# Kernel tuning notes

Measured on AMD Instinct MI355X. Metric: run time of the kernel, lower is better.

## Reference

```python
import jax, jax.numpy as jnp
import numpy as np

N_NODES = 50000
N_EDGES = 800000
N_GRAPHS = 256
D_IN, D_H1, D_H2, D_OUT = 64, 64, 64, 64


def gcn_conv(x, W, b, src, dst, n_nodes):
    # PyG GCNConv (eval): h = x @ W; add self-loops; deg[i] = in_deg(i) + 1;
    # out[i] = sum_{j->i} h[j] * deg[i]^-1/2 deg[j]^-1/2 + h[i]/deg[i] + b
    h = x @ W  # [N, F]
    ones = jnp.ones((src.shape[0],), dtype=x.dtype)
    deg = jax.ops.segment_sum(ones, dst, num_segments=n_nodes) + 1.0  # self loop
    dinv = jax.lax.rsqrt(deg)
    norm = dinv[src] * dinv[dst]  # [E]
    msg = h[src] * norm[:, None]  # [E, F]  (memory-bound gather)
    agg = jax.ops.segment_sum(msg, dst, num_segments=n_nodes)  # scatter-add
    agg = agg + h * (1.0 / deg)[:, None]  # self-loop contribution
    return agg + b


def setup_inputs() -> dict:
    key = jax.random.key(0)
    ks = jax.random.split(key, 12)
    x = jax.random.normal(ks[0], (N_NODES, D_IN), dtype=jnp.float32)
    src = jax.random.randint(ks[1], (N_EDGES,), 0, N_NODES)
    dst = jax.random.randint(ks[2], (N_EDGES,), 0, N_NODES)
    batch = jnp.sort(jax.random.randint(ks[3], (N_NODES,), 0, N_GRAPHS))
    def glorot(k, fin, fout):
        s = jnp.sqrt(6.0 / (fin + fout))
        return jax.random.uniform(k, (fin, fout), jnp.float32, -s, s)
    return {
        "x": x, "src": src, "dst": dst, "batch": batch,
        "W1": glorot(ks[4], D_IN, D_H1), "b1": jnp.zeros((D_H1,), jnp.float32),
        "W2": glorot(ks[5], D_H1, D_H2), "b2": jnp.zeros((D_H2,), jnp.float32),
        "W3": glorot(ks[6], D_H2, D_OUT), "b3": jnp.zeros((D_OUT,), jnp.float32),
        "Wl": glorot(ks[7], D_OUT, 1), "bl": jnp.zeros((1,), jnp.float32),
    }


def reference(x, src, dst, batch, W1, b1, W2, b2, W3, b3, Wl, bl):
    n = x.shape[0]
    h = jax.nn.relu(gcn_conv(x, W1, b1, src, dst, n))   # dropout inactive (eval)
    h = jax.nn.relu(gcn_conv(h, W2, b2, src, dst, n))
    h = jax.nn.relu(gcn_conv(h, W3, b3, src, dst, n))
    # global_mean_pool over graph ids
    sums = jax.ops.segment_sum(h, batch, num_segments=N_GRAPHS)  # [G, F]
    cnt = jax.ops.segment_sum(jnp.ones((n,), h.dtype), batch, num_segments=N_GRAPHS)
    pooled = sums / jnp.maximum(cnt, 1.0)[:, None]
    return pooled @ Wl + bl  # [G, 1]
```

## Files before the change

### kernel.cpp

```cpp
#include <hip/hip_runtime.h>

#define N_NODES 50000
#define N_EDGES 800000
#define N_GRAPHS 256
#define F 64
#define NBUCK 196
#define CAP 5120
#define P3_TILE 2048
#define P3_GRID ((N_EDGES + P3_TILE - 1) / P3_TILE)
#define BCAP 6144
#define ZOFF (N_NODES * 128)

__device__ __forceinline__ unsigned short f2bf(float f) {
    union { float f; unsigned u; } c; c.f = f;
    unsigned u = c.u + 0x7FFFu + ((c.u >> 16) & 1u);
    return (unsigned short)(u >> 16);
}
__device__ __forceinline__ unsigned pack2bf(float lo, float hi) {
    return (unsigned)f2bf(lo) | ((unsigned)f2bf(hi) << 16);
}
__device__ __forceinline__ float bfl(unsigned u) {
    union { unsigned u; float f; } c; c.u = u << 16; return c.f;
}
__device__ __forceinline__ float bfh(unsigned u) {
    union { unsigned u; float f; } c; c.u = u & 0xFFFF0000u; return c.f;
}

__global__ __launch_bounds__(256) void partition_edges(const int* __restrict__ src,
                                                       const int* __restrict__ dst,
                                                       int* __restrict__ bcur,
                                                       unsigned int* __restrict__ bpair) {
    __shared__ int bh[NBUCK], bloc[NBUCK], bpos[NBUCK];
    int t = threadIdx.x;
    int lo = blockIdx.x * P3_TILE;
    int hi = min(lo + P3_TILE, N_EDGES);
    for (int i = t; i < NBUCK; i += 256) { bh[i] = 0; bpos[i] = 0; }
    __syncthreads();
    for (int e = lo + t; e < hi; e += 256) atomicAdd(&bh[dst[e] >> 8], 1);
    __syncthreads();
    for (int i = t; i < NBUCK; i += 256)
        bloc[i] = bh[i] ? atomicAdd(&bcur[i], bh[i]) : 0;
    __syncthreads();
    for (int e = lo + t; e < hi; e += 256) {
        int d = dst[e];
        int b = d >> 8;
        int r = atomicAdd(&bpos[b], 1);
        bpair[(size_t)b * CAP + bloc[b] + r] = ((unsigned)src[e] << 8) | (unsigned)(d & 255);
    }
}

__global__ __launch_bounds__(256) void bucket_sort(const unsigned int* __restrict__ bpair,
                                                   const int* __restrict__ bcur,
                                                   int* __restrict__ eidx,
                                                   int* __restrict__ rbeg,
                                                   int* __restrict__ rend,
                                                   float* __restrict__ dinv,
                                                   unsigned short* __restrict__ Abf) {
    __shared__ int cnt[256], s[256], pos[256];
    __shared__ int lout[BCAP];
    int b = blockIdx.x, t = threadIdx.x;
    int base = b * CAP;
    int sz = bcur[b];

    if (b == 0 && t < 8) ((uint4*)Abf)[(size_t)N_NODES * 8 + t] = make_uint4(0u, 0u, 0u, 0u);

    cnt[t] = 0;
    __syncthreads();
    for (int i = t; i < sz; i += 256) atomicAdd(&cnt[bpair[base + i] & 255], 1);
    __syncthreads();
    int v = cnt[t];
    int pv = (v + 3) & ~3;
    s[t] = pv;
    __syncthreads();
    for (int off = 1; off < 256; off <<= 1) {
        int u = (t >= off) ? s[t - off] : 0;
        __syncthreads();
        s[t] += u;
        __syncthreads();
    }
    int excl = s[t] - pv;
    pos[t] = excl;
    int node = b * 256 + t;
    if (node < N_NODES) {
        rbeg[node] = base + excl;
        rend[node] = base + excl + pv;
        dinv[node] = 1.0f / sqrtf((float)v + 1.0f);
    }
    int padtot = s[255];
    __syncthreads();

    for (int i = t; i < sz; i += 256) {
        unsigned p = bpair[base + i];
        int r = atomicAdd(&pos[p & 255], 1);
        lout[r] = (int)((p >> 8) << 7);
    }
    __syncthreads();
    for (int j = v; j < pv; j++) lout[excl + j] = ZOFF;
    __syncthreads();
    for (int i = t; i < padtot; i += 256) eidx[base + i] = lout[i];
}

#define XSTRIDE 17
template <bool BF16IN>
__global__ __launch_bounds__(256) void gemm64_t(const void* __restrict__ Xv,
                                                const float* __restrict__ W,
                                                const float* __restrict__ dinv,
                                                unsigned short* __restrict__ Hn, int n) {
    __shared__ float4 sW[64 * 16];
    __shared__ float4 sX[128 * XSTRIDE];
    int tid = threadIdx.x;
    int base = blockIdx.x * 128;

    const float4* W4 = (const float4*)W;
    for (int i = tid; i < 64 * 16; i += 256) sW[i] = W4[i];
    if (BF16IN) {
        const uint4* X4 = (const uint4*)Xv;
        for (int i = tid; i < 128 * 8; i += 256) {
            int r = i >> 3, c = i & 7;
            int node = base + r;
            uint4 u = (node < n) ? X4[(size_t)node * 8 + c]
                                 : make_uint4(0u, 0u, 0u, 0u);
            sX[r * XSTRIDE + 2 * c]     = make_float4(bfl(u.x), bfh(u.x), bfl(u.y), bfh(u.y));
            sX[r * XSTRIDE + 2 * c + 1] = make_float4(bfl(u.z), bfh(u.z), bfl(u.w), bfh(u.w));
        }
    } else {
        const float4* X4 = (const float4*)Xv;
        for (int i = tid; i < 128 * 16; i += 256) {
            int r = i >> 4, kg = i & 15;
            int node = base + r;
            sX[r * XSTRIDE + kg] = (node < n) ? X4[(size_t)node * 16 + kg]
                                              : make_float4(0.f, 0.f, 0.f, 0.f);
        }
    }
    __syncthreads();

    int fg = tid & 15;
    int ng = tid >> 4;
    float4 acc[8];
#pragma unroll
    for (int ii = 0; ii < 8; ii++) acc[ii] = make_float4(0.f, 0.f, 0.f, 0.f);

    for (int kg = 0; kg < 16; kg++) {
        float4 xv[8];
#pragma unroll
        for (int ii = 0; ii < 8; ii++) xv[ii] = sX[(ng + 16 * ii) * XSTRIDE + kg];
#pragma unroll
        for (int kk = 0; kk < 4; kk++) {
            float4 wv = sW[(4 * kg + kk) * 16 + fg];
#pragma unroll
            for (int ii = 0; ii < 8; ii++) {
                float xs = (kk == 0) ? xv[ii].x : (kk == 1) ? xv[ii].y
                         : (kk == 2) ? xv[ii].z : xv[ii].w;
                acc[ii].x += wv.x * xs;
                acc[ii].y += wv.y * xs;
                acc[ii].z += wv.z * xs;
                acc[ii].w += wv.w * xs;
            }
        }
    }

    ushort4* H4 = (ushort4*)Hn;
#pragma unroll
    for (int ii = 0; ii < 8; ii++) {
        int node = base + ng + 16 * ii;
        if (node < n) {
            float d = dinv[node];
            float4 o = acc[ii];
            ushort4 u;
            u.x = f2bf(o.x * d); u.y = f2bf(o.y * d);
            u.z = f2bf(o.z * d); u.w = f2bf(o.w * d);
            H4[(size_t)node * 16 + fg] = u;
        }
    }
}

__global__ __launch_bounds__(256) void gather_layer(const int* __restrict__ rbeg,
                                                    const int* __restrict__ rend,
                                                    const int* __restrict__ eidx,
                                                    const float* __restrict__ dinv,
                                                    const unsigned short* __restrict__ Hn,
                                                    const float* __restrict__ b,
                                                    unsigned short* __restrict__ OUT, int n) {
    int wv = (blockIdx.x * blockDim.x + threadIdx.x) >> 6;
    int lane = threadIdx.x & 63;
    int ns = lane >> 3, f = lane & 7;
    int node = wv * 8 + ns;
    bool valid = node < n;
    int beg = valid ? rbeg[node] : 0;
    int end = valid ? rend[node] : 0;
    const char* Hb = (const char*)Hn;

    float a0 = 0.f, a1 = 0.f, a2 = 0.f, a3 = 0.f;
    float a4 = 0.f, a5 = 0.f, a6 = 0.f, a7 = 0.f;
    for (int k = beg; k < end; k += 4) {
        int4 o = *(const int4*)(eidx + k);
        uint4 p = *(const uint4*)(Hb + o.x + f * 16);
        uint4 q = *(const uint4*)(Hb + o.y + f * 16);
        uint4 r = *(const uint4*)(Hb + o.z + f * 16);
        uint4 w = *(const uint4*)(Hb + o.w + f * 16);
        a0 += (bfl(p.x) + bfl(q.x)) + (bfl(r.x) + bfl(w.x));
        a1 += (bfh(p.x) + bfh(q.x)) + (bfh(r.x) + bfh(w.x));
        a2 += (bfl(p.y) + bfl(q.y)) + (bfl(r.y) + bfl(w.y));
        a3 += (bfh(p.y) + bfh(q.y)) + (bfh(r.y) + bfh(w.y));
        a4 += (bfl(p.z) + bfl(q.z)) + (bfl(r.z) + bfl(w.z));
        a5 += (bfh(p.z) + bfh(q.z)) + (bfh(r.z) + bfh(w.z));
        a6 += (bfl(p.w) + bfl(q.w)) + (bfl(r.w) + bfl(w.w));
        a7 += (bfh(p.w) + bfh(q.w)) + (bfh(r.w) + bfh(w.w));
    }

    if (valid) {
        float di = dinv[node];
        uint4 hs = *(const uint4*)(Hb + (size_t)node * 128 + f * 16);
        float4 b0 = ((const float4*)b)[2 * f];
        float4 b1 = ((const float4*)b)[2 * f + 1];
        float v0 = fmaxf(di * (a0 + bfl(hs.x)) + b0.x, 0.f);
        float v1 = fmaxf(di * (a1 + bfh(hs.x)) + b0.y, 0.f);
        float v2 = fmaxf(di * (a2 + bfl(hs.y)) + b0.z, 0.f);
        float v3 = fmaxf(di * (a3 + bfh(hs.y)) + b0.w, 0.f);
        float v4 = fmaxf(di * (a4 + bfl(hs.z)) + b1.x, 0.f);
        float v5 = fmaxf(di * (a5 + bfh(hs.z)) + b1.y, 0.f);
        float v6 = fmaxf(di * (a6 + bfl(hs.w)) + b1.z, 0.f);
        float v7 = fmaxf(di * (a7 + bfh(hs.w)) + b1.w, 0.f);
        uint4 u;
        u.x = pack2bf(v0, v1); u.y = pack2bf(v2, v3);
        u.z = pack2bf(v4, v5); u.w = pack2bf(v6, v7);
        ((uint4*)OUT)[(size_t)node * 8 + f] = u;
    }
}

__global__ __launch_bounds__(256) void gather_pool(const int* __restrict__ rbeg,
                                                   const int* __restrict__ rend,
                                                   const int* __restrict__ eidx,
                                                   const float* __restrict__ dinv,
                                                   const unsigned short* __restrict__ Hn,
                                                   const float* __restrict__ b,
                                                   const float* __restrict__ Wl,
                                                   float* __restrict__ pdot, int n) {
    int wv = (blockIdx.x * blockDim.x + threadIdx.x) >> 6;
    int lane = threadIdx.x & 63;
    int ns = lane >> 3, f = lane & 7;
    int node = wv * 8 + ns;
    bool valid = node < n;
    int beg = valid ? rbeg[node] : 0;
    int end = valid ? rend[node] : 0;
    const char* Hb = (const char*)Hn;

    float a0 = 0.f, a1 = 0.f, a2 = 0.f, a3 = 0.f;
    float a4 = 0.f, a5 = 0.f, a6 = 0.f, a7 = 0.f;
    for (int k = beg; k < end; k += 4) {
        int4 o = *(const int4*)(eidx + k);
        uint4 p = *(const uint4*)(Hb + o.x + f * 16);
        uint4 q = *(const uint4*)(Hb + o.y + f * 16);
        uint4 r = *(const uint4*)(Hb + o.z + f * 16);
        uint4 w = *(const uint4*)(Hb + o.w + f * 16);
        a0 += (bfl(p.x) + bfl(q.x)) + (bfl(r.x) + bfl(w.x));
        a1 += (bfh(p.x) + bfh(q.x)) + (bfh(r.x) + bfh(w.x));
        a2 += (bfl(p.y) + bfl(q.y)) + (bfl(r.y) + bfl(w.y));
        a3 += (bfh(p.y) + bfh(q.y)) + (bfh(r.y) + bfh(w.y));
        a4 += (bfl(p.z) + bfl(q.z)) + (bfl(r.z) + bfl(w.z));
        a5 += (bfh(p.z) + bfh(q.z)) + (bfh(r.z) + bfh(w.z));
        a6 += (bfl(p.w) + bfl(q.w)) + (bfl(r.w) + bfl(w.w));
        a7 += (bfh(p.w) + bfh(q.w)) + (bfh(r.w) + bfh(w.w));
    }

    float di = valid ? dinv[node] : 0.f;
    uint4 hs = valid ? *(const uint4*)(Hb + (size_t)node * 128 + f * 16)
                     : make_uint4(0u, 0u, 0u, 0u);
    float4 b0 = ((const float4*)b)[2 * f];
    float4 b1 = ((const float4*)b)[2 * f + 1];
    float4 w0 = ((const float4*)Wl)[2 * f];
    float4 w1 = ((const float4*)Wl)[2 * f + 1];
    float d = 0.f;
    d += fmaxf(di * (a0 + bfl(hs.x)) + b0.x, 0.f) * w0.x;
    d += fmaxf(di * (a1 + bfh(hs.x)) + b0.y, 0.f) * w0.y;
    d += fmaxf(di * (a2 + bfl(hs.y)) + b0.z, 0.f) * w0.z;
    d += fmaxf(di * (a3 + bfh(hs.y)) + b0.w, 0.f) * w0.w;
    d += fmaxf(di * (a4 + bfl(hs.z)) + b1.x, 0.f) * w1.x;
    d += fmaxf(di * (a5 + bfh(hs.z)) + b1.y, 0.f) * w1.y;
    d += fmaxf(di * (a6 + bfl(hs.w)) + b1.z, 0.f) * w1.z;
    d += fmaxf(di * (a7 + bfh(hs.w)) + b1.w, 0.f) * w1.w;
#pragma unroll
    for (int m = 1; m <= 4; m <<= 1) d += __shfl_xor(d, m);
    if (valid && f == 0) pdot[node] = d;
}

__global__ __launch_bounds__(64) void final_out(const float* __restrict__ pdot,
                                                const int* __restrict__ batch,
                                                const float* __restrict__ bl,
                                                float* __restrict__ out) {
    int g = blockIdx.x;
    __shared__ int slo, shi;
    int lane = threadIdx.x;
    if (lane == 0) {
        int a = 0, b = N_NODES;
        while (a < b) { int m = (a + b) >> 1; if (batch[m] < g) a = m + 1; else b = m; }
        slo = a;
        b = N_NODES;
        while (a < b) { int m = (a + b) >> 1; if (batch[m] < g + 1) a = m + 1; else b = m; }
        shi = a;
    }
    __syncthreads();
    int lo = slo, hi = shi;
    float acc = 0.f;
    for (int i = lo + lane; i < hi; i += 64) acc += pdot[i];
#pragma unroll
    for (int off = 32; off > 0; off >>= 1) acc += __shfl_down(acc, off);
    if (lane == 0) {
        float cnt = (float)(hi - lo);
        out[g] = acc / fmaxf(cnt, 1.0f) + bl[0];
    }
}

extern "C" void kernel_launch(void* const* d_in, const int* in_sizes, int n_in,
                              void* d_out, int out_size, void* d_ws, size_t ws_size,
                              hipStream_t stream) {
    const float* x     = (const float*)d_in[0];
    const int*   src   = (const int*)d_in[1];
    const int*   dst   = (const int*)d_in[2];
    const int*   batch = (const int*)d_in[3];
    const float* W1 = (const float*)d_in[4];  const float* b1 = (const float*)d_in[5];
    const float* W2 = (const float*)d_in[6];  const float* b2 = (const float*)d_in[7];
    const float* W3 = (const float*)d_in[8];  const float* b3 = (const float*)d_in[9];
    const float* Wl = (const float*)d_in[10]; const float* bl = (const float*)d_in[11];
    float* out = (float*)d_out;

    char* ws = (char*)d_ws;
    unsigned short* Abf = (unsigned short*)ws;
    unsigned short* Bbf = Abf + (size_t)(N_NODES + 1) * F;
    float* dinv    = (float*)(Bbf + (size_t)N_NODES * F);
    float* pdot    = dinv + N_NODES;
    int*   rbeg    = (int*)(pdot + N_NODES);
    int*   rend    = rbeg + N_NODES;
    int*   bcur    = rend + N_NODES;
    unsigned int* bpair = (unsigned int*)(bcur + NBUCK);
    int*   eidx    = (int*)(bpair + (size_t)NBUCK * CAP);

    const int GEMM_GRID   = (N_NODES + 127) / 128;
    const int GATHER_GRID = (N_NODES + 31) / 32;

    hipMemsetAsync(bcur, 0, NBUCK * sizeof(int), stream);
    partition_edges<<<P3_GRID, 256, 0, stream>>>(src, dst, bcur, bpair);
    bucket_sort<<<NBUCK, 256, 0, stream>>>(bpair, bcur, eidx, rbeg, rend, dinv, Abf);

    gemm64_t<false><<<GEMM_GRID, 256, 0, stream>>>((const void*)x, W1, dinv, Abf, N_NODES);
    gather_layer<<<GATHER_GRID, 256, 0, stream>>>(rbeg, rend, eidx, dinv, Abf, b1, Bbf, N_NODES);

    gemm64_t<true><<<GEMM_GRID, 256, 0, stream>>>((const void*)Bbf, W2, dinv, Abf, N_NODES);
    gather_layer<<<GATHER_GRID, 256, 0, stream>>>(rbeg, rend, eidx, dinv, Abf, b2, Bbf, N_NODES);

    gemm64_t<true><<<GEMM_GRID, 256, 0, stream>>>((const void*)Bbf, W3, dinv, Abf, N_NODES);
    gather_pool<<<GATHER_GRID, 256, 0, stream>>>(rbeg, rend, eidx, dinv, Abf, b3, Wl, pdot, N_NODES);

    final_out<<<N_GRAPHS, 64, 0, stream>>>(pdot, batch, bl, out);
}
```

Measured before the change: 207.1 us.

## Fuse next-layer GEMM into gather epilogue using cross-lane bpermute

Replaces the separate bf16-input GEMM kernels for layers 2 and 3 with a gather kernel that, after aggregating and applying ReLU, multiplies the node's 64 features by the next layer's weights in registers. Features are exchanged across the 8 lanes of each node with ds_bpermute, and W is staged in shared memory. This removes two kernel launches and the extra read and write of the intermediate activations. In exchange, every gather block loads W into LDS and adds 64 bpermutes plus FMAs per lane. The two feature buffers now alternate, so both need a zero padding row and the dinv offset moves accordingly.

```diff
diff --git a/kernel.cpp b/kernel.cpp
--- a/kernel.cpp
+++ b/kernel.cpp
@@ -55,14 +55,18 @@
                                                    int* __restrict__ rbeg,
                                                    int* __restrict__ rend,
                                                    float* __restrict__ dinv,
-                                                   unsigned short* __restrict__ Abf) {
+                                                   unsigned short* __restrict__ Abf,
+                                                   unsigned short* __restrict__ Bbf) {
     __shared__ int cnt[256], s[256], pos[256];
     __shared__ int lout[BCAP];
     int b = blockIdx.x, t = threadIdx.x;
     int base = b * CAP;
     int sz = bcur[b];
 
-    if (b == 0 && t < 8) ((uint4*)Abf)[(size_t)N_NODES * 8 + t] = make_uint4(0u, 0u, 0u, 0u);
+    if (b == 0 && t < 8) {
+        ((uint4*)Abf)[(size_t)N_NODES * 8 + t] = make_uint4(0u, 0u, 0u, 0u);
+        ((uint4*)Bbf)[(size_t)N_NODES * 8 + t] = make_uint4(0u, 0u, 0u, 0u);
+    }
 
     cnt[t] = 0;
     __syncthreads();
@@ -101,11 +105,10 @@
 }
 
 #define XSTRIDE 17
-template <bool BF16IN>
-__global__ __launch_bounds__(256) void gemm64_t(const void* __restrict__ Xv,
-                                                const float* __restrict__ W,
-                                                const float* __restrict__ dinv,
-                                                unsigned short* __restrict__ Hn, int n) {
+__global__ __launch_bounds__(256) void gemm64_f32(const float* __restrict__ X,
+                                                  const float* __restrict__ W,
+                                                  const float* __restrict__ dinv,
+                                                  unsigned short* __restrict__ Hn, int n) {
     __shared__ float4 sW[64 * 16];
     __shared__ float4 sX[128 * XSTRIDE];
     int tid = threadIdx.x;
@@ -113,18 +116,8 @@
 
     const float4* W4 = (const float4*)W;
     for (int i = tid; i < 64 * 16; i += 256) sW[i] = W4[i];
-    if (BF16IN) {
-        const uint4* X4 = (const uint4*)Xv;
-        for (int i = tid; i < 128 * 8; i += 256) {
-            int r = i >> 3, c = i & 7;
-            int node = base + r;
-            uint4 u = (node < n) ? X4[(size_t)node * 8 + c]
-                                 : make_uint4(0u, 0u, 0u, 0u);
-            sX[r * XSTRIDE + 2 * c]     = make_float4(bfl(u.x), bfh(u.x), bfl(u.y), bfh(u.y));
-            sX[r * XSTRIDE + 2 * c + 1] = make_float4(bfl(u.z), bfh(u.z), bfl(u.w), bfh(u.w));
-        }
-    } else {
-        const float4* X4 = (const float4*)Xv;
+    {
+        const float4* X4 = (const float4*)X;
         for (int i = tid; i < 128 * 16; i += 256) {
             int r = i >> 4, kg = i & 15;
             int node = base + r;
@@ -174,21 +167,27 @@
     }
 }
 
-__global__ __launch_bounds__(256) void gather_layer(const int* __restrict__ rbeg,
-                                                    const int* __restrict__ rend,
-                                                    const int* __restrict__ eidx,
-                                                    const float* __restrict__ dinv,
-                                                    const unsigned short* __restrict__ Hn,
-                                                    const float* __restrict__ b,
-                                                    unsigned short* __restrict__ OUT, int n) {
+__global__ __launch_bounds__(256) void gather_gemm(const int* __restrict__ rbeg,
+                                                   const int* __restrict__ rend,
+                                                   const int* __restrict__ eidx,
+                                                   const float* __restrict__ dinv,
+                                                   const unsigned short* __restrict__ Hin,
+                                                   const float* __restrict__ bias,
+                                                   const float* __restrict__ W,
+                                                   unsigned short* __restrict__ Hout, int n) {
+    __shared__ float4 sW[64 * 16];
+    const float4* W4 = (const float4*)W;
+    for (int i = threadIdx.x; i < 64 * 16; i += 256) sW[i] = W4[i];
+    __syncthreads();
+
     int wv = (blockIdx.x * blockDim.x + threadIdx.x) >> 6;
+    if (wv * 8 >= n) return;
     int lane = threadIdx.x & 63;
     int ns = lane >> 3, f = lane & 7;
     int node = wv * 8 + ns;
-    bool valid = node < n;
-    int beg = valid ? rbeg[node] : 0;
-    int end = valid ? rend[node] : 0;
-    const char* Hb = (const char*)Hn;
+    int beg = rbeg[node];
+    int end = rend[node];
+    const char* Hb = (const char*)Hin;
 
     float a0 = 0.f, a1 = 0.f, a2 = 0.f, a3 = 0.f;
     float a4 = 0.f, a5 = 0.f, a6 = 0.f, a7 = 0.f;
@@ -208,24 +207,43 @@
         a7 += (bfh(p.w) + bfh(q.w)) + (bfh(r.w) + bfh(w.w));
     }
 
-    if (valid) {
-        float di = dinv[node];
-        uint4 hs = *(const uint4*)(Hb + (size_t)node * 128 + f * 16);
-        float4 b0 = ((const float4*)b)[2 * f];
-        float4 b1 = ((const float4*)b)[2 * f + 1];
-        float v0 = fmaxf(di * (a0 + bfl(hs.x)) + b0.x, 0.f);
-        float v1 = fmaxf(di * (a1 + bfh(hs.x)) + b0.y, 0.f);
-        float v2 = fmaxf(di * (a2 + bfl(hs.y)) + b0.z, 0.f);
-        float v3 = fmaxf(di * (a3 + bfh(hs.y)) + b0.w, 0.f);
-        float v4 = fmaxf(di * (a4 + bfl(hs.z)) + b1.x, 0.f);
-        float v5 = fmaxf(di * (a5 + bfh(hs.z)) + b1.y, 0.f);
-        float v6 = fmaxf(di * (a6 + bfl(hs.w)) + b1.z, 0.f);
-        float v7 = fmaxf(di * (a7 + bfh(hs.w)) + b1.w, 0.f);
-        uint4 u;
-        u.x = pack2bf(v0, v1); u.y = pack2bf(v2, v3);
-        u.z = pack2bf(v4, v5); u.w = pack2bf(v6, v7);
-        ((uint4*)OUT)[(size_t)node * 8 + f] = u;
-    }
+    float di = dinv[node];
+    uint4 hs = *(const uint4*)(Hb + (size_t)node * 128 + f * 16);
+    float4 bb0 = ((const float4*)bias)[2 * f];
+    float4 bb1 = ((const float4*)bias)[2 * f + 1];
+    float v[8];
+    v[0] = fmaxf(di * (a0 + bfl(hs.x)) + bb0.x, 0.f);
+    v[1] = fmaxf(di * (a1 + bfh(hs.x)) + bb0.y, 0.f);
+    v[2] = fmaxf(di * (a2 + bfl(hs.y)) + bb0.z, 0.f);
+    v[3] = fmaxf(di * (a3 + bfh(hs.y)) + bb0.w, 0.f);
+    v[4] = fmaxf(di * (a4 + bfl(hs.z)) + bb1.x, 0.f);
+    v[5] = fmaxf(di * (a5 + bfh(hs.z)) + bb1.y, 0.f);
+    v[6] = fmaxf(di * (a6 + bfl(hs.w)) + bb1.z, 0.f);
+    v[7] = fmaxf(di * (a7 + bfh(hs.w)) + bb1.w, 0.f);
+
+    float y0 = 0.f, y1 = 0.f, y2 = 0.f, y3 = 0.f;
+    float y4 = 0.f, y5 = 0.f, y6 = 0.f, y7 = 0.f;
+    int pb = (lane & 56) << 2;
+#pragma unroll
+    for (int c = 0; c < 8; ++c) {
+        int ad = pb + 4 * c;
+#pragma unroll
+        for (int j = 0; j < 8; ++j) {
+            float hk = __int_as_float(
+                __builtin_amdgcn_ds_bpermute(ad, __float_as_int(v[j])));
+            float4 w0 = sW[(8 * c + j) * 16 + 2 * f];
+            float4 w1 = sW[(8 * c + j) * 16 + 2 * f + 1];
+            y0 += hk * w0.x; y1 += hk * w0.y; y2 += hk * w0.z; y3 += hk * w0.w;
+            y4 += hk * w1.x; y5 += hk * w1.y; y6 += hk * w1.z; y7 += hk * w1.w;
+        }
+    }
+
+    uint4 u;
+    u.x = pack2bf(y0 * di, y1 * di);
+    u.y = pack2bf(y2 * di, y3 * di);
+    u.z = pack2bf(y4 * di, y5 * di);
+    u.w = pack2bf(y6 * di, y7 * di);
+    ((uint4*)Hout)[(size_t)node * 8 + f] = u;
 }
 
 __global__ __launch_bounds__(256) void gather_pool(const int* __restrict__ rbeg,
@@ -327,7 +345,7 @@
     char* ws = (char*)d_ws;
     unsigned short* Abf = (unsigned short*)ws;
     unsigned short* Bbf = Abf + (size_t)(N_NODES + 1) * F;
-    float* dinv    = (float*)(Bbf + (size_t)N_NODES * F);
+    float* dinv    = (float*)(Bbf + (size_t)(N_NODES + 1) * F);
     float* pdot    = dinv + N_NODES;
     int*   rbeg    = (int*)(pdot + N_NODES);
     int*   rend    = rbeg + N_NODES;
@@ -340,15 +358,14 @@
 
     hipMemsetAsync(bcur, 0, NBUCK * sizeof(int), stream);
     partition_edges<<<P3_GRID, 256, 0, stream>>>(src, dst, bcur, bpair);
-    bucket_sort<<<NBUCK, 256, 0, stream>>>(bpair, bcur, eidx, rbeg, rend, dinv, Abf);
-
-    gemm64_t<false><<<GEMM_GRID, 256, 0, stream>>>((const void*)x, W1, dinv, Abf, N_NODES);
-    gather_layer<<<GATHER_GRID, 256, 0, stream>>>(rbeg, rend, eidx, dinv, Abf, b1, Bbf, N_NODES);
-
-    gemm64_t<true><<<GEMM_GRID, 256, 0, stream>>>((const void*)Bbf, W2, dinv, Abf, N_NODES);
-    gather_layer<<<GATHER_GRID, 256, 0, stream>>>(rbeg, rend, eidx, dinv, Abf, b2, Bbf, N_NODES);
-
-    gemm64_t<true><<<GEMM_GRID, 256, 0, stream>>>((const void*)Bbf, W3, dinv, Abf, N_NODES);
+    bucket_sort<<<NBUCK, 256, 0, stream>>>(bpair, bcur, eidx, rbeg, rend, dinv, Abf, Bbf);
+
+    gemm64_f32<<<GEMM_GRID, 256, 0, stream>>>(x, W1, dinv, Abf, N_NODES);
+
+    gather_gemm<<<GATHER_GRID, 256, 0, stream>>>(rbeg, rend, eidx, dinv, Abf, b1, W2, Bbf, N_NODES);
+
+    gather_gemm<<<GATHER_GRID, 256, 0, stream>>>(rbeg, rend, eidx, dinv, Bbf, b2, W3, Abf, N_NODES);
+
     gather_pool<<<GATHER_GRID, 256, 0, stream>>>(rbeg, rend, eidx, dinv, Abf, b3, Wl, pdot, N_NODES);
 
     final_out<<<N_GRAPHS, 64, 0, stream>>>(pdot, batch, bl, out);
```

Result: faster. 195.7 us (-5.5%).
